# Optimization experiments

Hardware: AMD Instinct MI355X
Metric: run time of the kernel (lower is better)

The kernel has to match this reference:

```python
import jax, jax.numpy as jnp
import numpy as np

H = 512      # hidden_size
E = 300      # embedding_dim (word2vec)
V = 30000    # vocab size
C = 3        # num_classes
TP = 64      # premise max len
TH = 64      # hypothesis max len
B = 128      # batch


def setup_inputs() -> dict:
    key = jax.random.key(0)
    ks = jax.random.split(key, 20)
    def nrm(k, shape, scale=0.05):
        return jax.random.normal(k, shape, jnp.float32) * scale
    embed = nrm(ks[0], (V, E), 1.0).at[0].set(0.0)  # padding_idx=0 row zeroed
    return dict(
        premise=jax.random.randint(ks[1], (TP, B), 0, V),
        premise_len=jax.random.randint(ks[2], (B,), 1, TP),
        hypothesis=jax.random.randint(ks[3], (TH, B), 0, V),
        hypothesis_len=jax.random.randint(ks[4], (B,), 1, TH),
        embed=embed,
        w_e=jax.random.uniform(ks[5], (H,), jnp.float32),
        Ws=nrm(ks[6], (H, H)), Wt=nrm(ks[7], (H, H)), Wm=nrm(ks[8], (H, H)),
        Wih_p=nrm(ks[9], (4 * H, E)), bih_p=nrm(ks[10], (4 * H,)), bhh_p=nrm(ks[11], (4 * H,)),
        Wih_h=nrm(ks[12], (4 * H, E)), bih_h=nrm(ks[13], (4 * H,)), bhh_h=nrm(ks[14], (4 * H,)),
        Wih_m=nrm(ks[15], (4 * H, 2 * H)), bih_m=nrm(ks[16], (4 * H,)), bhh_m=nrm(ks[17], (4 * H,)),
        fc_w=nrm(ks[18], (C, H)), fc_b=nrm(ks[19], (C,)),
    )


def lstm_zero_state(x, Wih, bih, bhh):
    # PyTorch LSTMCell called with hx=None -> (h,c)=0, so weight_hh*h vanishes;
    # only bias_hh survives. Gate order: i, f, g, o.
    g = x @ Wih.T + bih + bhh
    i, f, gg, o = jnp.split(g, 4, axis=-1)
    c = jax.nn.sigmoid(i) * jnp.tanh(gg)
    return jax.nn.sigmoid(o) * jnp.tanh(c)


def reference(premise, premise_len, hypothesis, hypothesis_len, embed,
              w_e, Ws, Wt, Wm,
              Wih_p, bih_p, bhh_p,
              Wih_h, bih_h, bhh_h,
              Wih_m, bih_m, bhh_m,
              fc_w, fc_b):
    # Premise/hypothesis encoders: each timestep uses zero initial state (faithful).
    h_s = lstm_zero_state(embed[premise], Wih_p, bih_p, bhh_p)      # [TP, B, H]
    h_t = lstm_zero_state(embed[hypothesis], Wih_h, bih_h, bhh_h)   # [TH, B, H]
    pre_s = h_s @ Ws.T                                              # [TP, B, H]
    pre_t = h_t @ Wt.T                                              # [TH, B, H]

    def step(h_m_prev, xs):
        pt_k, ht_k = xs                                             # [B,H], [B,H]
        # additive attention: e[j,b] = w_e . tanh(Ws h_s + Wt h_t_k + Wm h_m_prev)
        scores = jnp.einsum('tbh,h->tb', jnp.tanh(pre_s + pt_k + h_m_prev @ Wm.T), w_e)
        alpha = jax.nn.softmax(scores, axis=0)                      # softmax over premise
        a_k = jnp.einsum('tb,tbh->bh', alpha, h_s)                  # [B, H]
        m_k = jnp.concatenate([a_k, ht_k], axis=1)                  # [B, 2H]
        h_m = lstm_zero_state(m_k, Wih_m, bih_m, bhh_m)             # match cell, zero state
        return h_m, None

    h0 = jnp.zeros((premise.shape[1], Ws.shape[0]), jnp.float32)
    h_m_final, _ = jax.lax.scan(step, h0, (pre_t, h_t))
    return h_m_final @ fc_w.T + fc_b                                # [B, C]
```

## Files before the change

kernel.cpp:

```cpp
#include <hip/hip_runtime.h>


#define DEV static __device__ __forceinline__

DEV float fast_sigmoid(float x) { return 1.0f / (1.0f + __expf(-x)); }
DEV float fast_tanh(float x)    { return 1.0f - 2.0f / (__expf(2.0f * x) + 1.0f); }

DEV unsigned f2bf(float x) {
    unsigned v = __float_as_uint(x);
    return (v + 0x7FFFu + ((v >> 16) & 1u)) >> 16;
}
DEV float blo(unsigned u) { return __uint_as_float(u << 16); }

DEV float ntload(const float* p) { return __builtin_nontemporal_load(p); }

typedef __attribute__((ext_vector_type(8))) short bfrag;
typedef __attribute__((ext_vector_type(4))) float ffrag;

#define G3_BLK_S 99328

DEV void cvt_hilo(const float* v, bfrag& hi, bfrag& lo)
{
#pragma unroll
    for (int z = 0; z < 8; ++z) {
        unsigned h = f2bf(v[z]);
        hi[z] = (short)h;
        lo[z] = (short)f2bf(v[z] - __uint_as_float(h << 16));
    }
}

__global__ __launch_bounds__(256, 2) void mfma_nt_kernel(
    const float* __restrict__ A, const float* __restrict__ W,
    float* __restrict__ C)
{
    const int wv   = threadIdx.x >> 6;
    const int lane = threadIdx.x & 63;
    const int row  = lane & 15;
    const int quad = lane >> 4;
    const int m0 = blockIdx.x * 256 + wv * 64;
    const int n0 = blockIdx.y * 64;

    ffrag acc[4][4];
#pragma unroll
    for (int mt = 0; mt < 4; ++mt)
#pragma unroll
        for (int n = 0; n < 4; ++n)
#pragma unroll
            for (int r = 0; r < 4; ++r) acc[mt][n][r] = 0.0f;

#pragma unroll 1
    for (int k0 = 0; k0 < 512; k0 += 32) {
        bfrag ahi[4], alo[4];
#pragma unroll
        for (int mt = 0; mt < 4; ++mt) {
            const float* ap = A + (size_t)(m0 + mt * 16 + row) * 512 + k0 + quad * 8;
            float4 aA = *(const float4*)ap;
            float4 aB = *(const float4*)(ap + 4);
            float av[8] = {aA.x, aA.y, aA.z, aA.w, aB.x, aB.y, aB.z, aB.w};
            cvt_hilo(av, ahi[mt], alo[mt]);
        }
#pragma unroll
        for (int n = 0; n < 4; ++n) {
            const float* wp = W + (size_t)(n0 + n * 16 + row) * 512 + k0 + quad * 8;
            float4 wA = *(const float4*)wp;
            float4 wB = *(const float4*)(wp + 4);
            float wvv[8] = {wA.x, wA.y, wA.z, wA.w, wB.x, wB.y, wB.z, wB.w};
            bfrag whi, wlo;
            cvt_hilo(wvv, whi, wlo);
#pragma unroll
            for (int mt = 0; mt < 4; ++mt) {
                acc[mt][n] = __builtin_amdgcn_mfma_f32_16x16x32_bf16(ahi[mt], whi, acc[mt][n], 0, 0, 0);
                acc[mt][n] = __builtin_amdgcn_mfma_f32_16x16x32_bf16(alo[mt], whi, acc[mt][n], 0, 0, 0);
                acc[mt][n] = __builtin_amdgcn_mfma_f32_16x16x32_bf16(ahi[mt], wlo, acc[mt][n], 0, 0, 0);
            }
        }
    }
#pragma unroll
    for (int mt = 0; mt < 4; ++mt)
#pragma unroll
        for (int n = 0; n < 4; ++n)
#pragma unroll
            for (int r = 0; r < 4; ++r)
                C[(size_t)(m0 + mt * 16 + quad * 4 + r) * 512 + n0 + n * 16 + row]
                    = acc[mt][n][r];
}

template<int GATHER>
__global__ __launch_bounds__(256, 2) void mfma_g3_kernel(
    const float* __restrict__ A, const int* __restrict__ gidx,
    int lda, int K,
    const float* __restrict__ W, int ldw,
    const float* __restrict__ bias1, const float* __restrict__ bias2,
    float* __restrict__ out)
{
    const int wv   = threadIdx.x >> 6;
    const int lane = threadIdx.x & 63;
    const int row  = lane & 15;
    const int quad = lane >> 4;
    const int m0   = blockIdx.x * 256 + wv * 64;
    const int gate = blockIdx.y >> 3;
    const int gbase = (gate == 0) ? 0 : (gate == 1 ? 1024 : 1536);
    const int j0   = (blockIdx.y & 7) * 64;

    int arow[4];
#pragma unroll
    for (int mt = 0; mt < 4; ++mt)
        arow[mt] = GATHER ? gidx[m0 + mt * 16 + row] : (m0 + mt * 16 + row);

    ffrag acc[4][4];
#pragma unroll
    for (int mt = 0; mt < 4; ++mt)
#pragma unroll
        for (int n = 0; n < 4; ++n)
#pragma unroll
            for (int r = 0; r < 4; ++r) acc[mt][n][r] = 0.0f;

#pragma unroll 1
    for (int k0 = 0; k0 < K; k0 += 32) {
        const bool tail = (k0 + 32 > K);
        bfrag ahi[4], alo[4];
#pragma unroll
        for (int mt = 0; mt < 4; ++mt) {
            float av[8];
            if (!tail) {
                const float* ap = A + (size_t)arow[mt] * lda + k0 + quad * 8;
                float4 aA = *(const float4*)ap;
                float4 aB = *(const float4*)(ap + 4);
                av[0]=aA.x; av[1]=aA.y; av[2]=aA.z; av[3]=aA.w;
                av[4]=aB.x; av[5]=aB.y; av[6]=aB.z; av[7]=aB.w;
            } else {
#pragma unroll
                for (int z = 0; z < 8; ++z) {
                    int kk = k0 + quad * 8 + z;
                    av[z] = (kk < K) ? A[(size_t)arow[mt] * lda + kk] : 0.0f;
                }
            }
            cvt_hilo(av, ahi[mt], alo[mt]);
        }
#pragma unroll
        for (int n = 0; n < 4; ++n) {
            const int wrow = gbase + j0 + n * 16 + row;
            float wvv[8];
            if (!tail) {
                const float* wp = W + (size_t)wrow * ldw + k0 + quad * 8;
                float4 wA = *(const float4*)wp;
                float4 wB = *(const float4*)(wp + 4);
                wvv[0]=wA.x; wvv[1]=wA.y; wvv[2]=wA.z; wvv[3]=wA.w;
                wvv[4]=wB.x; wvv[5]=wB.y; wvv[6]=wB.z; wvv[7]=wB.w;
            } else {
#pragma unroll
                for (int z = 0; z < 8; ++z) {
                    int kk = k0 + quad * 8 + z;
                    wvv[z] = (kk < K) ? W[(size_t)wrow * ldw + kk] : 0.0f;
                }
            }
            bfrag whi, wlo;
            cvt_hilo(wvv, whi, wlo);
#pragma unroll
            for (int mt = 0; mt < 4; ++mt) {
                acc[mt][n] = __builtin_amdgcn_mfma_f32_16x16x32_bf16(ahi[mt], whi, acc[mt][n], 0, 0, 0);
                acc[mt][n] = __builtin_amdgcn_mfma_f32_16x16x32_bf16(alo[mt], whi, acc[mt][n], 0, 0, 0);
                acc[mt][n] = __builtin_amdgcn_mfma_f32_16x16x32_bf16(ahi[mt], wlo, acc[mt][n], 0, 0, 0);
            }
        }
    }
#pragma unroll
    for (int n = 0; n < 4; ++n) {
        const int j = j0 + n * 16 + row;
        const float bb = bias1[gbase + j] + bias2[gbase + j];
#pragma unroll
        for (int mt = 0; mt < 4; ++mt)
#pragma unroll
            for (int r = 0; r < 4; ++r) {
                const int m = m0 + mt * 16 + quad * 4 + r;
                out[((size_t)m * 3 + gate) * 512 + j] = acc[mt][n][r] + bb;
            }
    }
}

__global__ __launch_bounds__(256, 2) void g3pack_kernel(
    const float* __restrict__ A,
    const float* __restrict__ W,
    unsigned short* __restrict__ G3s,
    int mbase)
{
    const int wv   = threadIdx.x >> 6;
    const int lane = threadIdx.x & 63;
    const int row  = lane & 15;
    const int quad = lane >> 4;
    const int m0   = blockIdx.x * 256 + wv * 64;
    const int gate = blockIdx.y >> 3;
    const int gbase = (gate == 0) ? 0 : (gate == 1 ? 1024 : 1536);
    const int j0   = (blockIdx.y & 7) * 64;

    ffrag acc[4][4];
#pragma unroll
    for (int mt = 0; mt < 4; ++mt)
#pragma unroll
        for (int n = 0; n < 4; ++n)
#pragma unroll
            for (int r = 0; r < 4; ++r) acc[mt][n][r] = 0.0f;

#pragma unroll 1
    for (int k0 = 0; k0 < 512; k0 += 32) {
        bfrag ahi[4], alo[4];
#pragma unroll
        for (int mt = 0; mt < 4; ++mt) {
            const float* ap = A + (size_t)(m0 + mt * 16 + row) * 512 + k0 + quad * 8;
            float4 aA = *(const float4*)ap;
            float4 aB = *(const float4*)(ap + 4);
            float av[8] = {aA.x, aA.y, aA.z, aA.w, aB.x, aB.y, aB.z, aB.w};
            cvt_hilo(av, ahi[mt], alo[mt]);
        }
#pragma unroll
        for (int n = 0; n < 4; ++n) {
            const int wrow = gbase + j0 + n * 16 + row;
            const float* wp = W + (size_t)wrow * 1024 + k0 + quad * 8;
            float4 wA = *(const float4*)wp;
            float4 wB = *(const float4*)(wp + 4);
            float wvv[8] = {wA.x, wA.y, wA.z, wA.w, wB.x, wB.y, wB.z, wB.w};
            bfrag whi, wlo;
            cvt_hilo(wvv, whi, wlo);
#pragma unroll
            for (int mt = 0; mt < 4; ++mt) {
                acc[mt][n] = __builtin_amdgcn_mfma_f32_16x16x32_bf16(ahi[mt], whi, acc[mt][n], 0, 0, 0);
                acc[mt][n] = __builtin_amdgcn_mfma_f32_16x16x32_bf16(alo[mt], whi, acc[mt][n], 0, 0, 0);
                acc[mt][n] = __builtin_amdgcn_mfma_f32_16x16x32_bf16(ahi[mt], wlo, acc[mt][n], 0, 0, 0);
            }
        }
    }
#pragma unroll
    for (int n = 0; n < 4; ++n) {
        const int j = j0 + n * 16 + row;
#pragma unroll
        for (int mt = 0; mt < 4; ++mt)
#pragma unroll
            for (int r = 0; r < 4; ++r) {
                const int mg = mbase + m0 + mt * 16 + quad * 4 + r;
                const int t = mg >> 7, b = mg & 127;
                size_t idx = (size_t)b * G3_BLK_S
                           + ((size_t)(gate * 512 + j)) * 64 + t;
                G3s[idx] = (unsigned short)f2bf(acc[mt][n][r]);
            }
    }
}

__global__ __launch_bounds__(256) void enc_gates_kernel(
    const float* __restrict__ P, float* __restrict__ h)
{
    const int i = blockIdx.x * 256 + threadIdx.x;
    const int m = i >> 7;
    const int j4 = (i & 127) * 4;
    const float* p = P + (size_t)m * 1536 + j4;
    float4 gi = *(const float4*)p;
    float4 gg = *(const float4*)(p + 512);
    float4 go = *(const float4*)(p + 1024);
    float4 r;
    r.x = fast_sigmoid(go.x) * fast_tanh(fast_sigmoid(gi.x) * fast_tanh(gg.x));
    r.y = fast_sigmoid(go.y) * fast_tanh(fast_sigmoid(gi.y) * fast_tanh(gg.y));
    r.z = fast_sigmoid(go.z) * fast_tanh(fast_sigmoid(gi.z) * fast_tanh(gg.z));
    r.w = fast_sigmoid(go.w) * fast_tanh(fast_sigmoid(gi.w) * fast_tanh(gg.w));
    *(float4*)&h[(size_t)m * 512 + j4] = r;
}

__global__ __launch_bounds__(256) void pack_wm_kernel(
    const float* __restrict__ Wm, unsigned* __restrict__ WmB)
{
    int i = blockIdx.x * 256 + threadIdx.x;
    int u = i & 3, lane = (i >> 2) & 63;
    int nt = (i >> 8) & 31, kc = i >> 13;
    int row = nt * 16 + (lane & 15);
    int k = kc * 32 + ((lane >> 4) << 3) + u * 2;
    unsigned lo = f2bf(Wm[(size_t)row * 512 + k]);
    unsigned hi = f2bf(Wm[(size_t)row * 512 + k + 1]);
    WmB[i] = lo | (hi << 16);
}

__global__ __launch_bounds__(1024) void phaseB_kernel(
    const float* __restrict__ pre_s, const float* __restrict__ pre_t,
    const float* __restrict__ pre_m_h,
    const unsigned* __restrict__ WmB, const unsigned short* __restrict__ G3s,
    const float* __restrict__ w_e,
    const float* __restrict__ fc_w,  const float* __restrict__ fc_b,
    float* __restrict__ out)
{
    extern __shared__ __align__(16) float psL[];
    __shared__ __align__(16) float hm[512];
    __shared__ __align__(16) float base[512];
    __shared__ __align__(16) float wesh[512];
    __shared__ __align__(16) float sc[64];
    __shared__ __align__(16) float red[2 * 512];
    __shared__ __align__(16) float gates3[1536];
    __shared__ __align__(16) unsigned short hmh[512];
    __shared__ __align__(16) unsigned short hml[512];
    __shared__ __align__(16) unsigned short sch[64];
    __shared__ __align__(16) unsigned short scl[64];

    const int b    = blockIdx.x;
    const int tid  = threadIdx.x;
    const int wv   = tid >> 6;
    const int lane = tid & 63;
    const int col  = lane & 15;
    const int quad = lane >> 4;

    if (tid < 512) {
        wesh[tid] = w_e[tid];
        hm[tid] = 0.0f; hmh[tid] = 0; hml[tid] = 0;
    }
    for (int i = tid; i < 32768; i += 1024) {
        int t = i >> 9, h = i & 511;
        psL[i] = ntload(&pre_s[((size_t)t * 128 + b) * 512 + h]);
    }
    __syncthreads();

    for (int k = 0; k < 64; ++k) {
        {
            const int kh2 = wv >> 3;
            const int tp  = (wv & 7) * 4;
            ffrag a0 = {0.0f,0.0f,0.0f,0.0f}, a1 = {0.0f,0.0f,0.0f,0.0f};
            ffrag a2 = {0.0f,0.0f,0.0f,0.0f}, a3 = {0.0f,0.0f,0.0f,0.0f};
            const uint4* wp = (const uint4*)WmB
                            + ((size_t)(kh2 * 8) * 32 + tp) * 64 + lane;
            const unsigned short* ab = ((lane & 8) == 0) ? hmh : hml;
#pragma unroll 1
            for (int kc = 0; kc < 8; ++kc) {
                bfrag a  = *(const bfrag*)&ab[(kh2 * 8 + kc) * 32 + quad * 8];
                bfrag w0 = *(const bfrag*)(wp);
                bfrag w1 = *(const bfrag*)(wp + 64);
                bfrag w2 = *(const bfrag*)(wp + 128);
                bfrag w3 = *(const bfrag*)(wp + 192);
                a0 = __builtin_amdgcn_mfma_f32_16x16x32_bf16(a, w0, a0, 0, 0, 0);
                a1 = __builtin_amdgcn_mfma_f32_16x16x32_bf16(a, w1, a1, 0, 0, 0);
                a2 = __builtin_amdgcn_mfma_f32_16x16x32_bf16(a, w2, a2, 0, 0, 0);
                a3 = __builtin_amdgcn_mfma_f32_16x16x32_bf16(a, w3, a3, 0, 0, 0);
                wp += 2048;
            }
            float s0 = a0[0] + __shfl_xor(a0[0], 32);
            float s1 = a1[0] + __shfl_xor(a1[0], 32);
            float s2 = a2[0] + __shfl_xor(a2[0], 32);
            float s3 = a3[0] + __shfl_xor(a3[0], 32);
            if (lane < 16) {
                float* rr = &red[kh2 * 512];
                rr[(tp + 0) * 16 + lane] = s0;
                rr[(tp + 1) * 16 + lane] = s1;
                rr[(tp + 2) * 16 + lane] = s2;
                rr[(tp + 3) * 16 + lane] = s3;
            }
        }
        __syncthreads();
        if (tid < 512)
            base[tid] = red[tid] + red[512 + tid]
                      + ntload(&pre_t[((size_t)k * 128 + b) * 512 + tid]);
        __syncthreads();

#pragma unroll
        for (int tt = 0; tt < 4; ++tt) {
            int t = wv * 4 + tt;
            const float* ps = &psL[t * 512];
            float p = 0.0f;
#pragma unroll
            for (int u = 0; u < 8; ++u) {
                int h = lane + 64 * u;
                p += wesh[h] * fast_tanh(ps[h] + base[h]);
            }
#pragma unroll
            for (int off = 32; off; off >>= 1) p += __shfl_xor(p, off);
            if (lane == 0) sc[t] = p;
        }
        __syncthreads();

        if (wv == 0) {
            float s = sc[lane], mx = s;
#pragma unroll
            for (int off = 32; off; off >>= 1) mx = fmaxf(mx, __shfl_xor(mx, off));
            float e = __expf(s - mx), sum = e;
#pragma unroll
            for (int off = 32; off; off >>= 1) sum += __shfl_xor(sum, off);
            float a = e / sum;
            unsigned hb = f2bf(a);
            sch[lane] = (unsigned short)hb;
            scl[lane] = (unsigned short)f2bf(a - blo(hb));
        }
        __syncthreads();

        {
            const unsigned short* ab = ((lane & 8) == 0) ? sch : scl;
            bfrag aA = *(const bfrag*)&ab[quad * 8];
            bfrag aB = *(const bfrag*)&ab[32 + quad * 8];
            const unsigned short* gp = G3s + (size_t)b * G3_BLK_S
                                     + ((size_t)(wv * 96) + col) * 64 + quad * 8;
            ffrag g[6];
#pragma unroll
            for (int t6 = 0; t6 < 6; ++t6) {
                g[t6][0] = 0.0f; g[t6][1] = 0.0f; g[t6][2] = 0.0f; g[t6][3] = 0.0f;
            }
#pragma unroll
            for (int t6 = 0; t6 < 6; ++t6) {
                bfrag w0 = *(const bfrag*)(gp + t6 * 1024);
                g[t6] = __builtin_amdgcn_mfma_f32_16x16x32_bf16(aA, w0, g[t6], 0, 0, 0);
            }
#pragma unroll
            for (int t6 = 0; t6 < 6; ++t6) {
                bfrag w1 = *(const bfrag*)(gp + t6 * 1024 + 32);
                g[t6] = __builtin_amdgcn_mfma_f32_16x16x32_bf16(aB, w1, g[t6], 0, 0, 0);
            }
#pragma unroll
            for (int t6 = 0; t6 < 6; ++t6) {
                float s = g[t6][0] + __shfl_xor(g[t6][0], 32);
                if (lane < 16) gates3[(wv * 6 + t6) * 16 + lane] = s;
            }
        }
        __syncthreads();

        if (tid < 512) {
            const size_t m = (size_t)k * 128 + b;
            float gi = gates3[tid]        + ntload(&pre_m_h[(m * 3 + 0) * 512 + tid]);
            float gg = gates3[512 + tid]  + ntload(&pre_m_h[(m * 3 + 1) * 512 + tid]);
            float go = gates3[1024 + tid] + ntload(&pre_m_h[(m * 3 + 2) * 512 + tid]);
            float cc = fast_sigmoid(gi) * fast_tanh(gg);
            float hv = fast_sigmoid(go) * fast_tanh(cc);
            hm[tid] = hv;
            unsigned hb = f2bf(hv);
            hmh[tid] = (unsigned short)hb;
            hml[tid] = (unsigned short)f2bf(hv - blo(hb));
        }
        __syncthreads();
    }

    if (wv < 3) {
        float p = 0.0f;
#pragma unroll
        for (int u = 0; u < 8; ++u) {
            int h = lane + 64 * u;
            p += hm[h] * fc_w[wv * 512 + h];
        }
#pragma unroll
        for (int off = 32; off; off >>= 1) p += __shfl_xor(p, off);
        if (lane == 0) out[b * 3 + wv] = p + fc_b[wv];
    }
}

extern "C" void kernel_launch(void* const* d_in, const int* in_sizes, int n_in,
                              void* d_out, int out_size, void* d_ws, size_t ws_size,
                              hipStream_t stream)
{
    (void)in_sizes; (void)n_in; (void)out_size;
    const int*   premise    = (const int*)d_in[0];
    const int*   hypothesis = (const int*)d_in[2];
    const float* embed  = (const float*)d_in[4];
    const float* w_e    = (const float*)d_in[5];
    const float* Ws     = (const float*)d_in[6];
    const float* Wt     = (const float*)d_in[7];
    const float* Wm     = (const float*)d_in[8];
    const float* Wih_p  = (const float*)d_in[9];
    const float* bih_p  = (const float*)d_in[10];
    const float* bhh_p  = (const float*)d_in[11];
    const float* Wih_h  = (const float*)d_in[12];
    const float* bih_h  = (const float*)d_in[13];
    const float* bhh_h  = (const float*)d_in[14];
    const float* Wih_m  = (const float*)d_in[15];
    const float* bih_m  = (const float*)d_in[16];
    const float* bhh_m  = (const float*)d_in[17];
    const float* fc_w   = (const float*)d_in[18];
    const float* fc_b   = (const float*)d_in[19];

    float* ws      = (float*)d_ws;
    float* Rh      = ws;
    float* pre_s   = ws + 2097152;
    float* pre_t   = ws + 6291456;
    float* pre_m_h = ws + 10485760;
    unsigned short* G3s = (unsigned short*)(ws + 23068672);
    unsigned* WmB  = (unsigned*)Rh;
    float* outp    = (float*)d_out;
    if (ws_size < (size_t)29556736 * 4) return;

    dim3 blk(256);

    for (int h = 0; h < 2; ++h) {
        float* P = pre_m_h + (size_t)h * 6291456;
        mfma_g3_kernel<1><<<dim3(16, 24), blk, 0, stream>>>(
            embed, premise + h * 4096, 300, 300, Wih_p, 300, bih_p, bhh_p, P);
        enc_gates_kernel<<<2048, blk, 0, stream>>>(P, Rh);
        mfma_nt_kernel<<<dim3(16, 8), blk, 0, stream>>>(
            Rh, Ws, pre_s + (size_t)h * 2097152);
        g3pack_kernel<<<dim3(16, 24), blk, 0, stream>>>(
            Rh, Wih_m, G3s, h * 4096);
    }
    for (int h = 0; h < 2; ++h) {
        float* P = pre_m_h + (size_t)h * 6291456;
        mfma_g3_kernel<1><<<dim3(16, 24), blk, 0, stream>>>(
            embed, hypothesis + h * 4096, 300, 300, Wih_h, 300, bih_h, bhh_h, P);
        enc_gates_kernel<<<2048, blk, 0, stream>>>(P, Rh);
        mfma_nt_kernel<<<dim3(16, 8), blk, 0, stream>>>(
            Rh, Wt, pre_t + (size_t)h * 2097152);
        mfma_g3_kernel<0><<<dim3(16, 24), blk, 0, stream>>>(
            Rh, nullptr, 512, 512, Wih_m + 512, 1024, bih_m, bhh_m,
            pre_m_h + (size_t)h * 6291456);
    }

    pack_wm_kernel<<<512, blk, 0, stream>>>(Wm, WmB);

    static int attr_done = 0;
    if (!attr_done) {
        hipFuncSetAttribute((const void*)phaseB_kernel,
                            hipFuncAttributeMaxDynamicSharedMemorySize, 131072);
        attr_done = 1;
    }
    phaseB_kernel<<<dim3(128), dim3(1024), 131072, stream>>>(
        pre_s, pre_t, pre_m_h, WmB, G3s, w_e, fc_w, fc_b, outp);
}
```

Baseline: 1.555 ms.

## Fuse encoder gather-GEMM with gate activations and merge downstream GEMMs into one kernel

The embedding gather GEMM now applies the LSTM gate nonlinearities in its epilogue and writes the hidden states as pre-split bf16 hi/lo fragments laid out in MFMA order. This removes the fp32 gate buffer round trip and the separate gate kernel. The Ws/Wt projection and the Wih_m GEMM are merged into one launch that reads those pre-converted A fragments, which also drops the repeated fp32-to-bf16 splitting. The cost is smaller tiles (128-thread blocks, 16-row gather tiles), which means more weight reloads per block.

```diff
diff --git a/kernel.cpp b/kernel.cpp
--- a/kernel.cpp
+++ b/kernel.cpp
@@ -29,16 +29,132 @@
     }
 }
 
-__global__ __launch_bounds__(256, 2) void mfma_nt_kernel(
-    const float* __restrict__ A, const float* __restrict__ W,
-    float* __restrict__ C)
+__global__ __launch_bounds__(128, 2) void gather_fused_kernel(
+    const float* __restrict__ embed, const int* __restrict__ gidx,
+    const float* __restrict__ Wih,
+    const float* __restrict__ bih, const float* __restrict__ bhh,
+    unsigned short* __restrict__ RhB)
 {
     const int wv   = threadIdx.x >> 6;
     const int lane = threadIdx.x & 63;
     const int row  = lane & 15;
     const int quad = lane >> 4;
-    const int m0 = blockIdx.x * 256 + wv * 64;
-    const int n0 = blockIdx.y * 64;
+    const int m0 = blockIdx.x * 32 + wv * 16;
+    const int j0 = blockIdx.y * 64;
+
+    const int arow = gidx[m0 + row];
+
+    ffrag acc[3][4];
+#pragma unroll
+    for (int g = 0; g < 3; ++g)
+#pragma unroll
+        for (int n = 0; n < 4; ++n)
+#pragma unroll
+            for (int r = 0; r < 4; ++r) acc[g][n][r] = 0.0f;
+
+#pragma unroll 1
+    for (int k0 = 0; k0 < 300; k0 += 32) {
+        const bool tail = (k0 + 32 > 300);
+        float av[8];
+        if (!tail) {
+            const float* ap = embed + (size_t)arow * 300 + k0 + quad * 8;
+            float4 aA = *(const float4*)ap;
+            float4 aB = *(const float4*)(ap + 4);
+            av[0]=aA.x; av[1]=aA.y; av[2]=aA.z; av[3]=aA.w;
+            av[4]=aB.x; av[5]=aB.y; av[6]=aB.z; av[7]=aB.w;
+        } else {
+#pragma unroll
+            for (int z = 0; z < 8; ++z) {
+                int kk = k0 + quad * 8 + z;
+                av[z] = (kk < 300) ? embed[(size_t)arow * 300 + kk] : 0.0f;
+            }
+        }
+        bfrag ahi, alo;
+        cvt_hilo(av, ahi, alo);
+#pragma unroll
+        for (int g = 0; g < 3; ++g) {
+            const int gbase = (g == 0) ? 0 : (g == 1 ? 1024 : 1536);
+#pragma unroll
+            for (int n = 0; n < 4; ++n) {
+                const int wrow = gbase + j0 + n * 16 + row;
+                float wvv[8];
+                if (!tail) {
+                    const float* wp = Wih + (size_t)wrow * 300 + k0 + quad * 8;
+                    float4 wA = *(const float4*)wp;
+                    float4 wB = *(const float4*)(wp + 4);
+                    wvv[0]=wA.x; wvv[1]=wA.y; wvv[2]=wA.z; wvv[3]=wA.w;
+                    wvv[4]=wB.x; wvv[5]=wB.y; wvv[6]=wB.z; wvv[7]=wB.w;
+                } else {
+#pragma unroll
+                    for (int z = 0; z < 8; ++z) {
+                        int kk = k0 + quad * 8 + z;
+                        wvv[z] = (kk < 300) ? Wih[(size_t)wrow * 300 + kk] : 0.0f;
+                    }
+                }
+                bfrag whi, wlo;
+                cvt_hilo(wvv, whi, wlo);
+                acc[g][n] = __builtin_amdgcn_mfma_f32_16x16x32_bf16(ahi, whi, acc[g][n], 0, 0, 0);
+                acc[g][n] = __builtin_amdgcn_mfma_f32_16x16x32_bf16(alo, whi, acc[g][n], 0, 0, 0);
+                acc[g][n] = __builtin_amdgcn_mfma_f32_16x16x32_bf16(ahi, wlo, acc[g][n], 0, 0, 0);
+            }
+        }
+    }
+
+#pragma unroll
+    for (int n = 0; n < 4; ++n) {
+        const int j = j0 + n * 16 + row;
+        const float b0 = bih[j]        + bhh[j];
+        const float b1 = bih[1024 + j] + bhh[1024 + j];
+        const float b2 = bih[1536 + j] + bhh[1536 + j];
+        const int kc     = j >> 5;
+        const int lane_g = ((j >> 3) & 3) * 16;
+        const int z      = j & 7;
+#pragma unroll
+        for (int r = 0; r < 4; ++r) {
+            const int m = m0 + quad * 4 + r;
+            float gi = acc[0][n][r] + b0;
+            float gg = acc[1][n][r] + b1;
+            float go = acc[2][n][r] + b2;
+            float cc = fast_sigmoid(gi) * fast_tanh(gg);
+            float hv = fast_sigmoid(go) * fast_tanh(cc);
+            size_t idx = ((size_t)(kc * 256 + (m >> 4)) * 64
+                          + lane_g + (m & 15)) * 16 + z;
+            unsigned hb = f2bf(hv);
+            RhB[idx]     = (unsigned short)hb;
+            RhB[idx + 8] = (unsigned short)f2bf(hv - blo(hb));
+        }
+    }
+}
+
+template<int HYP>
+__global__ __launch_bounds__(128, 2) void fusedA_kernel(
+    const uint4* __restrict__ AB,
+    const float* __restrict__ Wnt,
+    const float* __restrict__ Wg3,
+    const float* __restrict__ bias1, const float* __restrict__ bias2,
+    float* __restrict__ outNT,
+    unsigned short* __restrict__ G3s, int mbase,
+    float* __restrict__ outMH)
+{
+    const int wv   = threadIdx.x >> 6;
+    const int lane = threadIdx.x & 63;
+    const int row  = lane & 15;
+    const int quad = lane >> 4;
+    const int m0   = blockIdx.x * 128 + wv * 64;
+    const int mt0  = m0 >> 4;
+    const int yy   = blockIdx.y;
+    const bool isNT = (yy < 8);
+
+    int gate = 0, j0 = 0, gbase = 0, wbase, ldw;
+    const float* W;
+    if (isNT) {
+        W = Wnt; ldw = 512; wbase = yy * 64;
+    } else {
+        gate = (yy - 8) >> 3;
+        j0   = ((yy - 8) & 7) * 64;
+        gbase = (gate == 0) ? 0 : (gate == 1 ? 1024 : 1536);
+        W = Wg3; ldw = 1024; wbase = gbase + j0;
+    }
 
     ffrag acc[4][4];
 #pragma unroll
@@ -50,18 +166,18 @@
 
 #pragma unroll 1
     for (int k0 = 0; k0 < 512; k0 += 32) {
+        const int kc = k0 >> 5;
         bfrag ahi[4], alo[4];
 #pragma unroll
         for (int mt = 0; mt < 4; ++mt) {
-            const float* ap = A + (size_t)(m0 + mt * 16 + row) * 512 + k0 + quad * 8;
-            float4 aA = *(const float4*)ap;
-            float4 aB = *(const float4*)(ap + 4);
-            float av[8] = {aA.x, aA.y, aA.z, aA.w, aB.x, aB.y, aB.z, aB.w};
-            cvt_hilo(av, ahi[mt], alo[mt]);
+            const uint4* ap = AB + ((size_t)(kc * 256 + mt0 + mt) * 64 + lane) * 2;
+            ahi[mt] = *(const bfrag*)(ap);
+            alo[mt] = *(const bfrag*)(ap + 1);
         }
 #pragma unroll
         for (int n = 0; n < 4; ++n) {
-            const float* wp = W + (size_t)(n0 + n * 16 + row) * 512 + k0 + quad * 8;
+            const int wrow = wbase + n * 16 + row;
+            const float* wp = W + (size_t)wrow * ldw + k0 + quad * 8;
             float4 wA = *(const float4*)wp;
             float4 wB = *(const float4*)(wp + 4);
             float wvv[8] = {wA.x, wA.y, wA.z, wA.w, wB.x, wB.y, wB.z, wB.w};
@@ -75,192 +191,45 @@
             }
         }
     }
-#pragma unroll
-    for (int mt = 0; mt < 4; ++mt)
-#pragma unroll
-        for (int n = 0; n < 4; ++n)
-#pragma unroll
-            for (int r = 0; r < 4; ++r)
-                C[(size_t)(m0 + mt * 16 + quad * 4 + r) * 512 + n0 + n * 16 + row]
-                    = acc[mt][n][r];
-}
-
-template<int GATHER>
-__global__ __launch_bounds__(256, 2) void mfma_g3_kernel(
-    const float* __restrict__ A, const int* __restrict__ gidx,
-    int lda, int K,
-    const float* __restrict__ W, int ldw,
-    const float* __restrict__ bias1, const float* __restrict__ bias2,
-    float* __restrict__ out)
-{
-    const int wv   = threadIdx.x >> 6;
-    const int lane = threadIdx.x & 63;
-    const int row  = lane & 15;
-    const int quad = lane >> 4;
-    const int m0   = blockIdx.x * 256 + wv * 64;
-    const int gate = blockIdx.y >> 3;
-    const int gbase = (gate == 0) ? 0 : (gate == 1 ? 1024 : 1536);
-    const int j0   = (blockIdx.y & 7) * 64;
-
-    int arow[4];
-#pragma unroll
-    for (int mt = 0; mt < 4; ++mt)
-        arow[mt] = GATHER ? gidx[m0 + mt * 16 + row] : (m0 + mt * 16 + row);
-
-    ffrag acc[4][4];
-#pragma unroll
-    for (int mt = 0; mt < 4; ++mt)
-#pragma unroll
-        for (int n = 0; n < 4; ++n)
-#pragma unroll
-            for (int r = 0; r < 4; ++r) acc[mt][n][r] = 0.0f;
-
-#pragma unroll 1
-    for (int k0 = 0; k0 < K; k0 += 32) {
-        const bool tail = (k0 + 32 > K);
-        bfrag ahi[4], alo[4];
-#pragma unroll
-        for (int mt = 0; mt < 4; ++mt) {
-            float av[8];
-            if (!tail) {
-                const float* ap = A + (size_t)arow[mt] * lda + k0 + quad * 8;
-                float4 aA = *(const float4*)ap;
-                float4 aB = *(const float4*)(ap + 4);
-                av[0]=aA.x; av[1]=aA.y; av[2]=aA.z; av[3]=aA.w;
-                av[4]=aB.x; av[5]=aB.y; av[6]=aB.z; av[7]=aB.w;
-            } else {
-#pragma unroll
-                for (int z = 0; z < 8; ++z) {
-                    int kk = k0 + quad * 8 + z;
-                    av[z] = (kk < K) ? A[(size_t)arow[mt] * lda + kk] : 0.0f;
+
+    if (isNT) {
+#pragma unroll
+        for (int mt = 0; mt < 4; ++mt)
+#pragma unroll
+            for (int n = 0; n < 4; ++n)
+#pragma unroll
+                for (int r = 0; r < 4; ++r)
+                    outNT[(size_t)(m0 + mt * 16 + quad * 4 + r) * 512
+                          + wbase + n * 16 + row] = acc[mt][n][r];
+    } else if (!HYP) {
+#pragma unroll
+        for (int n = 0; n < 4; ++n) {
+            const int j = j0 + n * 16 + row;
+#pragma unroll
+            for (int mt = 0; mt < 4; ++mt)
+#pragma unroll
+                for (int r = 0; r < 4; ++r) {
+                    const int mg = mbase + m0 + mt * 16 + quad * 4 + r;
+                    const int t = mg >> 7, b = mg & 127;
+                    size_t idx = (size_t)b * G3_BLK_S
+                               + ((size_t)(gate * 512 + j)) * 64 + t;
+                    G3s[idx] = (unsigned short)f2bf(acc[mt][n][r]);
                 }
-            }
-            cvt_hilo(av, ahi[mt], alo[mt]);
-        }
+        }
+    } else {
 #pragma unroll
         for (int n = 0; n < 4; ++n) {
-            const int wrow = gbase + j0 + n * 16 + row;
-            float wvv[8];
-            if (!tail) {
-                const float* wp = W + (size_t)wrow * ldw + k0 + quad * 8;
-                float4 wA = *(const float4*)wp;
-                float4 wB = *(const float4*)(wp + 4);
-                wvv[0]=wA.x; wvv[1]=wA.y; wvv[2]=wA.z; wvv[3]=wA.w;
-                wvv[4]=wB.x; wvv[5]=wB.y; wvv[6]=wB.z; wvv[7]=wB.w;
-            } else {
-#pragma unroll
-                for (int z = 0; z < 8; ++z) {
-                    int kk = k0 + quad * 8 + z;
-                    wvv[z] = (kk < K) ? W[(size_t)wrow * ldw + kk] : 0.0f;
+            const int j = j0 + n * 16 + row;
+            const float bb = bias1[gbase + j] + bias2[gbase + j];
+#pragma unroll
+            for (int mt = 0; mt < 4; ++mt)
+#pragma unroll
+                for (int r = 0; r < 4; ++r) {
+                    const int m = m0 + mt * 16 + quad * 4 + r;
+                    outMH[((size_t)m * 3 + gate) * 512 + j] = acc[mt][n][r] + bb;
                 }
-            }
-            bfrag whi, wlo;
-            cvt_hilo(wvv, whi, wlo);
-#pragma unroll
-            for (int mt = 0; mt < 4; ++mt) {
-                acc[mt][n] = __builtin_amdgcn_mfma_f32_16x16x32_bf16(ahi[mt], whi, acc[mt][n], 0, 0, 0);
-                acc[mt][n] = __builtin_amdgcn_mfma_f32_16x16x32_bf16(alo[mt], whi, acc[mt][n], 0, 0, 0);
-                acc[mt][n] = __builtin_amdgcn_mfma_f32_16x16x32_bf16(ahi[mt], wlo, acc[mt][n], 0, 0, 0);
-            }
-        }
-    }
-#pragma unroll
-    for (int n = 0; n < 4; ++n) {
-        const int j = j0 + n * 16 + row;
-        const float bb = bias1[gbase + j] + bias2[gbase + j];
-#pragma unroll
-        for (int mt = 0; mt < 4; ++mt)
-#pragma unroll
-            for (int r = 0; r < 4; ++r) {
-                const int m = m0 + mt * 16 + quad * 4 + r;
-                out[((size_t)m * 3 + gate) * 512 + j] = acc[mt][n][r] + bb;
-            }
-    }
-}
-
-__global__ __launch_bounds__(256, 2) void g3pack_kernel(
-    const float* __restrict__ A,
-    const float* __restrict__ W,
-    unsigned short* __restrict__ G3s,
-    int mbase)
-{
-    const int wv   = threadIdx.x >> 6;
-    const int lane = threadIdx.x & 63;
-    const int row  = lane & 15;
-    const int quad = lane >> 4;
-    const int m0   = blockIdx.x * 256 + wv * 64;
-    const int gate = blockIdx.y >> 3;
-    const int gbase = (gate == 0) ? 0 : (gate == 1 ? 1024 : 1536);
-    const int j0   = (blockIdx.y & 7) * 64;
-
-    ffrag acc[4][4];
-#pragma unroll
-    for (int mt = 0; mt < 4; ++mt)
-#pragma unroll
-        for (int n = 0; n < 4; ++n)
-#pragma unroll
-            for (int r = 0; r < 4; ++r) acc[mt][n][r] = 0.0f;
-
-#pragma unroll 1
-    for (int k0 = 0; k0 < 512; k0 += 32) {
-        bfrag ahi[4], alo[4];
-#pragma unroll
-        for (int mt = 0; mt < 4; ++mt) {
-            const float* ap = A + (size_t)(m0 + mt * 16 + row) * 512 + k0 + quad * 8;
-            float4 aA = *(const float4*)ap;
-            float4 aB = *(const float4*)(ap + 4);
-            float av[8] = {aA.x, aA.y, aA.z, aA.w, aB.x, aB.y, aB.z, aB.w};
-            cvt_hilo(av, ahi[mt], alo[mt]);
-        }
-#pragma unroll
-        for (int n = 0; n < 4; ++n) {
-            const int wrow = gbase + j0 + n * 16 + row;
-            const float* wp = W + (size_t)wrow * 1024 + k0 + quad * 8;
-            float4 wA = *(const float4*)wp;
-            float4 wB = *(const float4*)(wp + 4);
-            float wvv[8] = {wA.x, wA.y, wA.z, wA.w, wB.x, wB.y, wB.z, wB.w};
-            bfrag whi, wlo;
-            cvt_hilo(wvv, whi, wlo);
-#pragma unroll
-            for (int mt = 0; mt < 4; ++mt) {
-                acc[mt][n] = __builtin_amdgcn_mfma_f32_16x16x32_bf16(ahi[mt], whi, acc[mt][n], 0, 0, 0);
-                acc[mt][n] = __builtin_amdgcn_mfma_f32_16x16x32_bf16(alo[mt], whi, acc[mt][n], 0, 0, 0);
-                acc[mt][n] = __builtin_amdgcn_mfma_f32_16x16x32_bf16(ahi[mt], wlo, acc[mt][n], 0, 0, 0);
-            }
-        }
-    }
-#pragma unroll
-    for (int n = 0; n < 4; ++n) {
-        const int j = j0 + n * 16 + row;
-#pragma unroll
-        for (int mt = 0; mt < 4; ++mt)
-#pragma unroll
-            for (int r = 0; r < 4; ++r) {
-                const int mg = mbase + m0 + mt * 16 + quad * 4 + r;
-                const int t = mg >> 7, b = mg & 127;
-                size_t idx = (size_t)b * G3_BLK_S
-                           + ((size_t)(gate * 512 + j)) * 64 + t;
-                G3s[idx] = (unsigned short)f2bf(acc[mt][n][r]);
-            }
-    }
-}
-
-__global__ __launch_bounds__(256) void enc_gates_kernel(
-    const float* __restrict__ P, float* __restrict__ h)
-{
-    const int i = blockIdx.x * 256 + threadIdx.x;
-    const int m = i >> 7;
-    const int j4 = (i & 127) * 4;
-    const float* p = P + (size_t)m * 1536 + j4;
-    float4 gi = *(const float4*)p;
-    float4 gg = *(const float4*)(p + 512);
-    float4 go = *(const float4*)(p + 1024);
-    float4 r;
-    r.x = fast_sigmoid(go.x) * fast_tanh(fast_sigmoid(gi.x) * fast_tanh(gg.x));
-    r.y = fast_sigmoid(go.y) * fast_tanh(fast_sigmoid(gi.y) * fast_tanh(gg.y));
-    r.z = fast_sigmoid(go.z) * fast_tanh(fast_sigmoid(gi.z) * fast_tanh(gg.z));
-    r.w = fast_sigmoid(go.w) * fast_tanh(fast_sigmoid(gi.w) * fast_tanh(gg.w));
-    *(float4*)&h[(size_t)m * 512 + j4] = r;
+        }
+    }
 }
 
 __global__ __launch_bounds__(256) void pack_wm_kernel(
@@ -465,36 +434,32 @@
     const float* fc_b   = (const float*)d_in[19];
 
     float* ws      = (float*)d_ws;
-    float* Rh      = ws;
+    unsigned short* RhB = (unsigned short*)ws;
+    const uint4* RhB4   = (const uint4*)ws;
     float* pre_s   = ws + 2097152;
     float* pre_t   = ws + 6291456;
     float* pre_m_h = ws + 10485760;
     unsigned short* G3s = (unsigned short*)(ws + 23068672);
-    unsigned* WmB  = (unsigned*)Rh;
+    unsigned* WmB  = (unsigned*)ws;
     float* outp    = (float*)d_out;
     if (ws_size < (size_t)29556736 * 4) return;
 
+    dim3 blk2(128);
     dim3 blk(256);
 
     for (int h = 0; h < 2; ++h) {
-        float* P = pre_m_h + (size_t)h * 6291456;
-        mfma_g3_kernel<1><<<dim3(16, 24), blk, 0, stream>>>(
-            embed, premise + h * 4096, 300, 300, Wih_p, 300, bih_p, bhh_p, P);
-        enc_gates_kernel<<<2048, blk, 0, stream>>>(P, Rh);
-        mfma_nt_kernel<<<dim3(16, 8), blk, 0, stream>>>(
-            Rh, Ws, pre_s + (size_t)h * 2097152);
-        g3pack_kernel<<<dim3(16, 24), blk, 0, stream>>>(
-            Rh, Wih_m, G3s, h * 4096);
+        gather_fused_kernel<<<dim3(128, 8), blk2, 0, stream>>>(
+            embed, premise + h * 4096, Wih_p, bih_p, bhh_p, RhB);
+        fusedA_kernel<0><<<dim3(32, 32), blk2, 0, stream>>>(
+            RhB4, Ws, Wih_m, nullptr, nullptr,
+            pre_s + (size_t)h * 2097152, G3s, h * 4096, nullptr);
     }
     for (int h = 0; h < 2; ++h) {
-        float* P = pre_m_h + (size_t)h * 6291456;
-        mfma_g3_kernel<1><<<dim3(16, 24), blk, 0, stream>>>(
-            embed, hypothesis + h * 4096, 300, 300, Wih_h, 300, bih_h, bhh_h, P);
-        enc_gates_kernel<<<2048, blk, 0, stream>>>(P, Rh);
-        mfma_nt_kernel<<<dim3(16, 8), blk, 0, stream>>>(
-            Rh, Wt, pre_t + (size_t)h * 2097152);
-        mfma_g3_kernel<0><<<dim3(16, 24), blk, 0, stream>>>(
-            Rh, nullptr, 512, 512, Wih_m + 512, 1024, bih_m, bhh_m,
+        gather_fused_kernel<<<dim3(128, 8), blk2, 0, stream>>>(
+            embed, hypothesis + h * 4096, Wih_h, bih_h, bhh_h, RhB);
+        fusedA_kernel<1><<<dim3(32, 32), blk2, 0, stream>>>(
+            RhB4, Wt, Wih_m + 512, bih_m, bhh_m,
+            pre_t + (size_t)h * 2097152, nullptr, 0,
             pre_m_h + (size_t)h * 6291456);
     }
 
```

Result: faster. 1.316 ms (-15.4%).
